# Optimization experiments

Measured on AMD Instinct MI355X. Metric: run time of the kernel, lower is better.

## Reference

```python
import jax, jax.numpy as jnp
import numpy as np

CLASS_COUNT = 100
IN_FEATURES = 256
OUT_FEATURES = 256


def setup_inputs() -> dict:
    key = jax.random.key(0)
    k1, k2, k3, k4 = jax.random.split(key, 4)
    N, C, H, W = 32, IN_FEATURES, 64, 64
    x = jax.random.normal(k1, (N, C, H, W), dtype=jnp.float32)
    classes = jax.random.randint(k2, (N,), 0, CLASS_COUNT, dtype=jnp.int32)
    # kaiming_uniform_(a=sqrt(5)) on [class_count, out, in]: fan_in = in_features
    fan_in = IN_FEATURES
    gain = np.sqrt(2.0 / (1.0 + 5.0))  # leaky_relu gain with a=sqrt(5)
    wbound = gain * np.sqrt(3.0 / fan_in)
    weight = jax.random.uniform(k3, (CLASS_COUNT, OUT_FEATURES, IN_FEATURES),
                                dtype=jnp.float32, minval=-wbound, maxval=wbound)
    bbound = 1.0 / np.sqrt(fan_in)
    bias = jax.random.uniform(k4, (CLASS_COUNT, OUT_FEATURES),
                              dtype=jnp.float32, minval=-bbound, maxval=bbound)
    return {"x": x, "classes": classes, "weight": weight, "bias": bias}


def reference(x, classes, weight, bias):
    # Per-sample weight/bias gather then 1x1 conv == batched matmul over pixels.
    w = weight[classes]          # [N, O, C]
    b = bias[classes]            # [N, O]
    out = jnp.einsum('nchw,noc->nohw', x, w)
    return out + b[:, :, None, None]
```

## Files before the change

kernel.cpp:

```cpp
#include <hip/hip_runtime.h>

#define CIN    256
#define COUT   256
#define PTOT   4096
#define BN     64
#define BK     32
#define KSTEPS 8
#define LDSK   48

typedef __attribute__((ext_vector_type(8)))  short bfrag;
typedef __attribute__((ext_vector_type(16))) float f32x16;

__device__ __forceinline__ unsigned int f2bf(float f) {
    unsigned int x = __float_as_uint(f);
    x += 0x7fffu + ((x >> 16) & 1u);
    return x >> 16;
}

__device__ __forceinline__ int swz(int row, int k) {
    return k ^ (((row >> 2) & 3) << 3);
}

__device__ __forceinline__ f32x16 zero16() {
    f32x16 v;
    #pragma unroll
    for (int i = 0; i < 16; ++i) v[i] = 0.0f;
    return v;
}

__global__ __launch_bounds__(256, 2)
void selconv_mfma(const float* __restrict__ x,
                  const int*   __restrict__ classes,
                  const float* __restrict__ weight,
                  const float* __restrict__ bias,
                  float*       __restrict__ out)
{
    __shared__ unsigned short As[2][COUT * LDSK];
    __shared__ unsigned short Bs[2][BN * LDSK];
    __shared__ float bias_s[COUT];

    const int b     = blockIdx.x;
    const int xcd   = b & 7;
    const int local = b >> 3;
    const int n     = xcd * 4 + (local >> 6);
    const int pt    = local & 63;
    const int p0    = pt * BN;

    const int tid  = threadIdx.x;
    const int lane = tid & 63;
    const int wid  = tid >> 6;

    const int cls = classes[n];
    const float* Wn = weight + (size_t)cls * (COUT * CIN);
    const float* Xn = x   + (size_t)n * (CIN * PTOT) + p0;
    float*       On = out + (size_t)n * (COUT * PTOT) + p0;

    bias_s[tid] = bias[cls * COUT + tid];

    const int a_row0 = tid >> 3;
    const int a_col  = (tid & 7) * 4;
    const int b_k2   = (tid >> 4) * 2;
    const int b_p4   = (tid & 15) * 4;

    float4 av[8];
    float4 bva, bvb;

    auto load_tile = [&](int t) {
        const int k0 = t * BK;
        #pragma unroll
        for (int i = 0; i < 8; ++i)
            av[i] = *(const float4*)(Wn + (size_t)(a_row0 + 32 * i) * CIN + k0 + a_col);
        bva = *(const float4*)(Xn + (size_t)(k0 + b_k2)     * PTOT + b_p4);
        bvb = *(const float4*)(Xn + (size_t)(k0 + b_k2 + 1) * PTOT + b_p4);
    };

    auto write_tile = [&](int buf) {
        #pragma unroll
        for (int i = 0; i < 8; ++i) {
            const int row = a_row0 + 32 * i;
            uint2 w;
            w.x = f2bf(av[i].x) | (f2bf(av[i].y) << 16);
            w.y = f2bf(av[i].z) | (f2bf(av[i].w) << 16);
            *(uint2*)(&As[buf][row * LDSK + swz(row, a_col)]) = w;
        }
        const float pa[4] = {bva.x, bva.y, bva.z, bva.w};
        const float pb[4] = {bvb.x, bvb.y, bvb.z, bvb.w};
        #pragma unroll
        for (int i = 0; i < 4; ++i) {
            const int p = b_p4 + i;
            unsigned int w = f2bf(pa[i]) | (f2bf(pb[i]) << 16);
            *(unsigned int*)(&Bs[buf][p * LDSK + swz(p, b_k2)]) = w;
        }
    };

    const int fr  = lane & 31;
    const int fg8 = (lane >> 5) * 8;
    f32x16 acc00 = zero16(), acc01 = zero16(), acc10 = zero16(), acc11 = zero16();

    load_tile(0);
    write_tile(0);
    __syncthreads();

    for (int t = 0; t < KSTEPS; ++t) {
        const int buf = t & 1;
        if (t + 1 < KSTEPS) load_tile(t + 1);

        const unsigned short* Ab = As[buf];
        const unsigned short* Bb = Bs[buf];
        const int rowA0 = wid * 64 + fr;
        #pragma unroll
        for (int s = 0; s < 2; ++s) {
            const int kof = s * 16 + fg8;
            bfrag a0 = *(const bfrag*)(&Ab[(rowA0     ) * LDSK + swz(rowA0,      kof)]);
            bfrag a1 = *(const bfrag*)(&Ab[(rowA0 + 32) * LDSK + swz(rowA0 + 32, kof)]);
            bfrag b0 = *(const bfrag*)(&Bb[(fr     ) * LDSK + swz(fr,      kof)]);
            bfrag b1 = *(const bfrag*)(&Bb[(fr + 32) * LDSK + swz(fr + 32, kof)]);
            acc00 = __builtin_amdgcn_mfma_f32_32x32x16_bf16(a0, b0, acc00, 0, 0, 0);
            acc01 = __builtin_amdgcn_mfma_f32_32x32x16_bf16(a0, b1, acc01, 0, 0, 0);
            acc10 = __builtin_amdgcn_mfma_f32_32x32x16_bf16(a1, b0, acc10, 0, 0, 0);
            acc11 = __builtin_amdgcn_mfma_f32_32x32x16_bf16(a1, b1, acc11, 0, 0, 0);
        }

        if (t + 1 < KSTEPS) write_tile(buf ^ 1);
        __syncthreads();
    }

    const int col = lane & 31;
    const int rh  = (lane >> 5) * 4;

    auto store_frag = [&](f32x16 a, int mi, int nj) {
        const int ob = wid * 64 + mi * 32;
        const int pc = nj * 32 + col;
        #pragma unroll
        for (int r = 0; r < 16; ++r) {
            const int row = (r & 3) + 8 * (r >> 2) + rh;
            const int o   = ob + row;
            On[(size_t)o * PTOT + pc] = a[r] + bias_s[o];
        }
    };
    store_frag(acc00, 0, 0);
    store_frag(acc01, 0, 1);
    store_frag(acc10, 1, 0);
    store_frag(acc11, 1, 1);
}

extern "C" void kernel_launch(void* const* d_in, const int* in_sizes, int n_in,
                              void* d_out, int out_size, void* d_ws, size_t ws_size,
                              hipStream_t stream) {
    const float* x       = (const float*)d_in[0];
    const int*   classes = (const int*)d_in[1];
    const float* weight  = (const float*)d_in[2];
    const float* bias    = (const float*)d_in[3];
    float*       out     = (float*)d_out;

    const int grid = 32 * (PTOT / BN);
    selconv_mfma<<<grid, 256, 0, stream>>>(x, classes, weight, bias, out);
}
```

Baseline: 76.80 us.

## Retile to 128x128 output tiles with 2x2 wave layout and deeper prefetch

Changes each block's tile from all 256 output channels by 64 pixels to 128 channels by 128 pixels, with four waves arranged 2x2. Global loads now use two register sets so tiles t+2 and t+3 are fetched while MFMA work runs on the current LDS buffer. Occupancy in launch_bounds rises from 2 to 3 blocks. The aim is to cut weight reloads, LDS use and register pressure. The cost is that each x slice is now read by two blocks, which relies on L2 hits.

```diff
diff --git a/kernel.cpp b/kernel.cpp
--- a/kernel.cpp
+++ b/kernel.cpp
@@ -3,7 +3,8 @@
 #define CIN    256
 #define COUT   256
 #define PTOT   4096
-#define BN     64
+#define BM     128
+#define BN     128
 #define BK     32
 #define KSTEPS 8
 #define LDSK   48
@@ -28,68 +29,81 @@
     return v;
 }
 
-__global__ __launch_bounds__(256, 2)
+__global__ __launch_bounds__(256, 3)
 void selconv_mfma(const float* __restrict__ x,
                   const int*   __restrict__ classes,
                   const float* __restrict__ weight,
                   const float* __restrict__ bias,
                   float*       __restrict__ out)
 {
-    __shared__ unsigned short As[2][COUT * LDSK];
+    __shared__ unsigned short As[2][BM * LDSK];
     __shared__ unsigned short Bs[2][BN * LDSK];
-    __shared__ float bias_s[COUT];
+    __shared__ float bias_s[BM];
 
     const int b     = blockIdx.x;
     const int xcd   = b & 7;
     const int local = b >> 3;
     const int n     = xcd * 4 + (local >> 6);
-    const int pt    = local & 63;
-    const int p0    = pt * BN;
+    const int rem   = local & 63;
+    const int o0    = (rem >> 5) * BM;
+    const int p0    = (rem & 31) * BN;
 
     const int tid  = threadIdx.x;
     const int lane = tid & 63;
     const int wid  = tid >> 6;
+    const int wr   = wid >> 1;
+    const int wc   = wid & 1;
 
     const int cls = classes[n];
-    const float* Wn = weight + (size_t)cls * (COUT * CIN);
+    const float* Wn = weight + (size_t)cls * (COUT * CIN) + (size_t)o0 * CIN;
     const float* Xn = x   + (size_t)n * (CIN * PTOT) + p0;
-    float*       On = out + (size_t)n * (COUT * PTOT) + p0;
+    float*       On = out + (size_t)n * (COUT * PTOT) + (size_t)o0 * PTOT + p0;
 
-    bias_s[tid] = bias[cls * COUT + tid];
+    if (tid < BM) bias_s[tid] = bias[cls * COUT + o0 + tid];
 
     const int a_row0 = tid >> 3;
     const int a_col  = (tid & 7) * 4;
-    const int b_k2   = (tid >> 4) * 2;
-    const int b_p4   = (tid & 15) * 4;
+    const int b_p4   = (tid & 31) * 4;
+    const int b_kp   = (tid >> 5) * 2;
 
-    float4 av[8];
-    float4 bva, bvb;
+    float4 A0[4], A1[4];
+    float4 B0[4], B1[4];
 
-    auto load_tile = [&](int t) {
+    auto loadA = [&](float4 (&A)[4], int t) {
         const int k0 = t * BK;
         #pragma unroll
-        for (int i = 0; i < 8; ++i)
-            av[i] = *(const float4*)(Wn + (size_t)(a_row0 + 32 * i) * CIN + k0 + a_col);
-        bva = *(const float4*)(Xn + (size_t)(k0 + b_k2)     * PTOT + b_p4);
-        bvb = *(const float4*)(Xn + (size_t)(k0 + b_k2 + 1) * PTOT + b_p4);
+        for (int i = 0; i < 4; ++i)
+            A[i] = *(const float4*)(Wn + (size_t)(a_row0 + 32 * i) * CIN + k0 + a_col);
     };
-
-    auto write_tile = [&](int buf) {
+    auto loadB = [&](float4 (&B)[4], int t) {
+        const int k0 = t * BK;
         #pragma unroll
-        for (int i = 0; i < 8; ++i) {
+        for (int j = 0; j < 2; ++j) {
+            const int kr = k0 + b_kp + 16 * j;
+            B[j * 2 + 0] = *(const float4*)(Xn + (size_t)kr       * PTOT + b_p4);
+            B[j * 2 + 1] = *(const float4*)(Xn + (size_t)(kr + 1) * PTOT + b_p4);
+        }
+    };
+    auto writeT = [&](int buf, float4 (&A)[4], float4 (&B)[4]) {
+        #pragma unroll
+        for (int i = 0; i < 4; ++i) {
             const int row = a_row0 + 32 * i;
             uint2 w;
-            w.x = f2bf(av[i].x) | (f2bf(av[i].y) << 16);
-            w.y = f2bf(av[i].z) | (f2bf(av[i].w) << 16);
+            w.x = f2bf(A[i].x) | (f2bf(A[i].y) << 16);
+            w.y = f2bf(A[i].z) | (f2bf(A[i].w) << 16);
             *(uint2*)(&As[buf][row * LDSK + swz(row, a_col)]) = w;
         }
-        const float pa[4] = {bva.x, bva.y, bva.z, bva.w};
-        const float pb[4] = {bvb.x, bvb.y, bvb.z, bvb.w};
         #pragma unroll
-        for (int i = 0; i < 4; ++i) {
-            const int p = b_p4 + i;
-            unsigned int w = f2bf(pa[i]) | (f2bf(pb[i]) << 16);
-            *(unsigned int*)(&Bs[buf][p * LDSK + swz(p, b_k2)]) = w;
+        for (int j = 0; j < 2; ++j) {
+            const int kk = b_kp + 16 * j;
+            const float pa[4] = {B[j*2+0].x, B[j*2+0].y, B[j*2+0].z, B[j*2+0].w};
+            const float pb[4] = {B[j*2+1].x, B[j*2+1].y, B[j*2+1].z, B[j*2+1].w};
+            #pragma unroll
+            for (int i = 0; i < 4; ++i) {
+                const int p = b_p4 + i;
+                const unsigned int w = f2bf(pa[i]) | (f2bf(pb[i]) << 16);
+                *(unsigned int*)(&Bs[buf][p * LDSK + swz(p, kk)]) = w;
+            }
         }
     };
 
@@ -97,40 +111,47 @@
     const int fg8 = (lane >> 5) * 8;
     f32x16 acc00 = zero16(), acc01 = zero16(), acc10 = zero16(), acc11 = zero16();
 
-    load_tile(0);
-    write_tile(0);
-    __syncthreads();
-
-    for (int t = 0; t < KSTEPS; ++t) {
-        const int buf = t & 1;
-        if (t + 1 < KSTEPS) load_tile(t + 1);
-
+    auto mfma_step = [&](int buf) {
         const unsigned short* Ab = As[buf];
         const unsigned short* Bb = Bs[buf];
-        const int rowA0 = wid * 64 + fr;
+        const int rowA0 = wr * 64 + fr;
+        const int colB0 = wc * 64 + fr;
         #pragma unroll
         for (int s = 0; s < 2; ++s) {
             const int kof = s * 16 + fg8;
             bfrag a0 = *(const bfrag*)(&Ab[(rowA0     ) * LDSK + swz(rowA0,      kof)]);
             bfrag a1 = *(const bfrag*)(&Ab[(rowA0 + 32) * LDSK + swz(rowA0 + 32, kof)]);
-            bfrag b0 = *(const bfrag*)(&Bb[(fr     ) * LDSK + swz(fr,      kof)]);
-            bfrag b1 = *(const bfrag*)(&Bb[(fr + 32) * LDSK + swz(fr + 32, kof)]);
+            bfrag b0 = *(const bfrag*)(&Bb[(colB0     ) * LDSK + swz(colB0,      kof)]);
+            bfrag b1 = *(const bfrag*)(&Bb[(colB0 + 32) * LDSK + swz(colB0 + 32, kof)]);
             acc00 = __builtin_amdgcn_mfma_f32_32x32x16_bf16(a0, b0, acc00, 0, 0, 0);
             acc01 = __builtin_amdgcn_mfma_f32_32x32x16_bf16(a0, b1, acc01, 0, 0, 0);
             acc10 = __builtin_amdgcn_mfma_f32_32x32x16_bf16(a1, b0, acc10, 0, 0, 0);
             acc11 = __builtin_amdgcn_mfma_f32_32x32x16_bf16(a1, b1, acc11, 0, 0, 0);
         }
+    };
 
-        if (t + 1 < KSTEPS) write_tile(buf ^ 1);
+    loadA(A0, 0); loadB(B0, 0);
+    loadA(A1, 1); loadB(B1, 1);
+    writeT(0, A0, B0);
+    __syncthreads();
+
+    #pragma unroll
+    for (int t = 0; t < KSTEPS; t += 2) {
+        if (t + 2 < KSTEPS) { loadA(A0, t + 2); loadB(B0, t + 2); }
+        mfma_step(0);
+        writeT(1, A1, B1);
         __syncthreads();
+        if (t + 3 < KSTEPS) { loadA(A1, t + 3); loadB(B1, t + 3); }
+        mfma_step(1);
+        if (t + 2 < KSTEPS) { writeT(0, A0, B0); __syncthreads(); }
     }
 
     const int col = lane & 31;
     const int rh  = (lane >> 5) * 4;
 
     auto store_frag = [&](f32x16 a, int mi, int nj) {
-        const int ob = wid * 64 + mi * 32;
-        const int pc = nj * 32 + col;
+        const int ob = wr * 64 + mi * 32;
+        const int pc = wc * 64 + nj * 32 + col;
         #pragma unroll
         for (int r = 0; r < 16; ++r) {
             const int row = (r & 3) + 8 * (r >> 2) + rh;
@@ -153,6 +174,6 @@
     const float* bias    = (const float*)d_in[3];
     float*       out     = (float*)d_out;
 
-    const int grid = 32 * (PTOT / BN);
+    const int grid = 32 * (COUT / BM) * (PTOT / BN);
     selconv_mfma<<<grid, 256, 0, stream>>>(x, classes, weight, bias, out);
 }
```

New measurement: 62.83 us. 1.22x faster.

## Load MFMA fragments directly from global memory, dropping LDS staging

Applied to the files above, without the earlier changes.

Removes the shared-memory double buffer and builds bf16 MFMA operands directly from global loads in registers, using the packed v_cvt_pk_bf16_f32 instruction for conversion. The block grows to 512 threads with 8 waves in a 4x2 arrangement, each wave computing a 64x32 tile with two accumulators, and loads are software-pipelined across K chunks. This eliminates LDS writes, reads and barriers, at the cost of redundant global loads across waves. The B operand now uses strided scalar loads (stride PTOT per element), and the whole block no longer shares one staged copy of the weight tile.

```diff
diff --git a/kernel.cpp b/kernel.cpp
--- a/kernel.cpp
+++ b/kernel.cpp
@@ -4,21 +4,33 @@
 #define COUT   256
 #define PTOT   4096
 #define BN     64
-#define BK     32
-#define KSTEPS 8
-#define LDSK   48
 
 typedef __attribute__((ext_vector_type(8)))  short bfrag;
 typedef __attribute__((ext_vector_type(16))) float f32x16;
 
-__device__ __forceinline__ unsigned int f2bf(float f) {
-    unsigned int x = __float_as_uint(f);
-    x += 0x7fffu + ((x >> 16) & 1u);
-    return x >> 16;
+__device__ __forceinline__ unsigned int cvt_pk(float lo, float hi) {
+    unsigned int r;
+    asm("v_cvt_pk_bf16_f32 %0, %1, %2" : "=v"(r) : "v"(lo), "v"(hi));
+    return r;
 }
 
-__device__ __forceinline__ int swz(int row, int k) {
-    return k ^ (((row >> 2) & 3) << 3);
+union FragU { unsigned int u[4]; bfrag f; };
+
+__device__ __forceinline__ bfrag mk_fragA(const float4 lo, const float4 hi) {
+    FragU r;
+    r.u[0] = cvt_pk(lo.x, lo.y);
+    r.u[1] = cvt_pk(lo.z, lo.w);
+    r.u[2] = cvt_pk(hi.x, hi.y);
+    r.u[3] = cvt_pk(hi.z, hi.w);
+    return r.f;
+}
+__device__ __forceinline__ bfrag mk_fragB(const float* bb) {
+    FragU r;
+    r.u[0] = cvt_pk(bb[0], bb[1]);
+    r.u[1] = cvt_pk(bb[2], bb[3]);
+    r.u[2] = cvt_pk(bb[4], bb[5]);
+    r.u[3] = cvt_pk(bb[6], bb[7]);
+    return r.f;
 }
 
 __device__ __forceinline__ f32x16 zero16() {
@@ -28,120 +40,79 @@
     return v;
 }
 
-__global__ __launch_bounds__(256, 2)
-void selconv_mfma(const float* __restrict__ x,
-                  const int*   __restrict__ classes,
-                  const float* __restrict__ weight,
-                  const float* __restrict__ bias,
-                  float*       __restrict__ out)
+__global__ __launch_bounds__(512, 4)
+void selconv_direct(const float* __restrict__ x,
+                    const int*   __restrict__ classes,
+                    const float* __restrict__ weight,
+                    const float* __restrict__ bias,
+                    float*       __restrict__ out)
 {
-    __shared__ unsigned short As[2][COUT * LDSK];
-    __shared__ unsigned short Bs[2][BN * LDSK];
-    __shared__ float bias_s[COUT];
-
     const int b     = blockIdx.x;
     const int xcd   = b & 7;
     const int local = b >> 3;
     const int n     = xcd * 4 + (local >> 6);
-    const int pt    = local & 63;
-    const int p0    = pt * BN;
+    const int p0    = (local & 63) * BN;
 
     const int tid  = threadIdx.x;
     const int lane = tid & 63;
     const int wid  = tid >> 6;
+    const int wr   = wid >> 1;
+    const int wc   = wid & 1;
+
+    const int fr = lane & 31;
+    const int kh = (lane >> 5) * 8;
 
     const int cls = classes[n];
-    const float* Wn = weight + (size_t)cls * (COUT * CIN);
-    const float* Xn = x   + (size_t)n * (CIN * PTOT) + p0;
-    float*       On = out + (size_t)n * (COUT * PTOT) + p0;
+    const float* Wn  = weight + (size_t)cls * (COUT * CIN);
+    const float* Xc  = x + (size_t)n * (CIN * PTOT) + p0 + wc * 32 + fr;
+    const float* A0p = Wn + (size_t)(wr * 64 + fr) * CIN + kh;
+    const float* A1p = A0p + 32 * CIN;
 
-    bias_s[tid] = bias[cls * COUT + tid];
+    f32x16 acc0 = zero16(), acc1 = zero16();
 
-    const int a_row0 = tid >> 3;
-    const int a_col  = (tid & 7) * 4;
-    const int b_k2   = (tid >> 4) * 2;
-    const int b_p4   = (tid & 15) * 4;
+    float4 a0l0, a0h0, a1l0, a1h0, a0l1, a0h1, a1l1, a1h1;
+    float  bb0[8], bb1[8];
 
-    float4 av[8];
-    float4 bva, bvb;
-
-    auto load_tile = [&](int t) {
-        const int k0 = t * BK;
+    auto loadS = [&](float4& p, float4& q, float4& r_, float4& s_,
+                     float (&bb)[8], int c) {
+        const int k0 = c * 16;
+        p  = *(const float4*)(A0p + k0);
+        q  = *(const float4*)(A0p + k0 + 4);
+        r_ = *(const float4*)(A1p + k0);
+        s_ = *(const float4*)(A1p + k0 + 4);
         #pragma unroll
-        for (int i = 0; i < 8; ++i)
-            av[i] = *(const float4*)(Wn + (size_t)(a_row0 + 32 * i) * CIN + k0 + a_col);
-        bva = *(const float4*)(Xn + (size_t)(k0 + b_k2)     * PTOT + b_p4);
-        bvb = *(const float4*)(Xn + (size_t)(k0 + b_k2 + 1) * PTOT + b_p4);
+        for (int j = 0; j < 8; ++j)
+            bb[j] = Xc[(k0 + kh + j) * PTOT];
     };
 
-    auto write_tile = [&](int buf) {
-        #pragma unroll
-        for (int i = 0; i < 8; ++i) {
-            const int row = a_row0 + 32 * i;
-            uint2 w;
-            w.x = f2bf(av[i].x) | (f2bf(av[i].y) << 16);
-            w.y = f2bf(av[i].z) | (f2bf(av[i].w) << 16);
-            *(uint2*)(&As[buf][row * LDSK + swz(row, a_col)]) = w;
+    loadS(a0l0, a0h0, a1l0, a1h0, bb0, 0);
+    #pragma unroll
+    for (int c = 0; c < 16; c += 2) {
+        loadS(a0l1, a0h1, a1l1, a1h1, bb1, c + 1);
+        {
+            const bfrag bf = mk_fragB(bb0);
+            acc0 = __builtin_amdgcn_mfma_f32_32x32x16_bf16(mk_fragA(a0l0, a0h0), bf, acc0, 0, 0, 0);
+            acc1 = __builtin_amdgcn_mfma_f32_32x32x16_bf16(mk_fragA(a1l0, a1h0), bf, acc1, 0, 0, 0);
         }
-        const float pa[4] = {bva.x, bva.y, bva.z, bva.w};
-        const float pb[4] = {bvb.x, bvb.y, bvb.z, bvb.w};
-        #pragma unroll
-        for (int i = 0; i < 4; ++i) {
-            const int p = b_p4 + i;
-            unsigned int w = f2bf(pa[i]) | (f2bf(pb[i]) << 16);
-            *(unsigned int*)(&Bs[buf][p * LDSK + swz(p, b_k2)]) = w;
+        if (c + 2 < 16) loadS(a0l0, a0h0, a1l0, a1h0, bb0, c + 2);
+        {
+            const bfrag bf = mk_fragB(bb1);
+            acc0 = __builtin_amdgcn_mfma_f32_32x32x16_bf16(mk_fragA(a0l1, a0h1), bf, acc0, 0, 0, 0);
+            acc1 = __builtin_amdgcn_mfma_f32_32x32x16_bf16(mk_fragA(a1l1, a1h1), bf, acc1, 0, 0, 0);
         }
-    };
-
-    const int fr  = lane & 31;
-    const int fg8 = (lane >> 5) * 8;
-    f32x16 acc00 = zero16(), acc01 = zero16(), acc10 = zero16(), acc11 = zero16();
-
-    load_tile(0);
-    write_tile(0);
-    __syncthreads();
-
-    for (int t = 0; t < KSTEPS; ++t) {
-        const int buf = t & 1;
-        if (t + 1 < KSTEPS) load_tile(t + 1);
-
-        const unsigned short* Ab = As[buf];
-        const unsigned short* Bb = Bs[buf];
-        const int rowA0 = wid * 64 + fr;
-        #pragma unroll
-        for (int s = 0; s < 2; ++s) {
-            const int kof = s * 16 + fg8;
-            bfrag a0 = *(const bfrag*)(&Ab[(rowA0     ) * LDSK + swz(rowA0,      kof)]);
-            bfrag a1 = *(const bfrag*)(&Ab[(rowA0 + 32) * LDSK + swz(rowA0 + 32, kof)]);
-            bfrag b0 = *(const bfrag*)(&Bb[(fr     ) * LDSK + swz(fr,      kof)]);
-            bfrag b1 = *(const bfrag*)(&Bb[(fr + 32) * LDSK + swz(fr + 32, kof)]);
-            acc00 = __builtin_amdgcn_mfma_f32_32x32x16_bf16(a0, b0, acc00, 0, 0, 0);
-            acc01 = __builtin_amdgcn_mfma_f32_32x32x16_bf16(a0, b1, acc01, 0, 0, 0);
-            acc10 = __builtin_amdgcn_mfma_f32_32x32x16_bf16(a1, b0, acc10, 0, 0, 0);
-            acc11 = __builtin_amdgcn_mfma_f32_32x32x16_bf16(a1, b1, acc11, 0, 0, 0);
-        }
-
-        if (t + 1 < KSTEPS) write_tile(buf ^ 1);
-        __syncthreads();
     }
 
-    const int col = lane & 31;
-    const int rh  = (lane >> 5) * 4;
-
-    auto store_frag = [&](f32x16 a, int mi, int nj) {
-        const int ob = wid * 64 + mi * 32;
-        const int pc = nj * 32 + col;
-        #pragma unroll
-        for (int r = 0; r < 16; ++r) {
-            const int row = (r & 3) + 8 * (r >> 2) + rh;
-            const int o   = ob + row;
-            On[(size_t)o * PTOT + pc] = a[r] + bias_s[o];
-        }
-    };
-    store_frag(acc00, 0, 0);
-    store_frag(acc01, 0, 1);
-    store_frag(acc10, 1, 0);
-    store_frag(acc11, 1, 1);
+    const float* bp = bias + cls * COUT;
+    float* On = out + (size_t)n * (COUT * PTOT) + p0 + wc * 32 + fr;
+    const int rh = (lane >> 5) * 4;
+    const int ob = wr * 64;
+    #pragma unroll
+    for (int r = 0; r < 16; ++r) {
+        const int row = (r & 3) + 8 * (r >> 2) + rh;
+        const int o0r = ob + row;
+        On[(size_t)o0r * PTOT]        = acc0[r] + bp[o0r];
+        On[(size_t)(o0r + 32) * PTOT] = acc1[r] + bp[o0r + 32];
+    }
 }
 
 extern "C" void kernel_launch(void* const* d_in, const int* in_sizes, int n_in,
@@ -154,5 +125,5 @@
     float*       out     = (float*)d_out;
 
     const int grid = 32 * (PTOT / BN);
-    selconv_mfma<<<grid, 256, 0, stream>>>(x, classes, weight, bias, out);
+    selconv_direct<<<grid, 512, 0, stream>>>(x, classes, weight, bias, out);
 }
```

Result: slower. 165.2 us (+115.1%).
